# Kernel optimization log

Hardware: AMD Instinct MI355X
Metric: run time of the kernel (lower is better)

## Reference

```python
import jax, jax.numpy as jnp
from jax import lax
import numpy as np

N = 10000      # nodes
E = 160000     # edges (avg degree 16)
IN = 128       # in_channels
H = 64         # hidden_channels
OUT = 112      # out_channels
L = 28         # num GENConv layers
LN_EPS = 1e-5
MSG_EPS = 1e-7   # GENConv adds eps after relu in message
SM_EPS = 1e-16   # PyG scatter-softmax denominator eps


def _ln(x, g, b):
    mu = jnp.mean(x, axis=-1, keepdims=True)
    var = jnp.mean(jnp.square(x - mu), axis=-1, keepdims=True)
    return (x - mu) * lax.rsqrt(var + LN_EPS) * g + b


def setup_inputs() -> dict:
    key = jax.random.key(0)
    ks = jax.random.split(key, 8)

    def w(k, shape, fan_in):
        return (jax.random.normal(k, shape, dtype=jnp.float32) / np.float32(np.sqrt(fan_in)))

    x = jax.random.normal(ks[0], (N, IN), dtype=jnp.float32)
    edge_index = jax.random.randint(ks[1], (2, E), 0, N, dtype=jnp.int32)

    inp = {
        "x": x,
        "edge_index": edge_index,
        # node encoder
        "enc_W": w(ks[2], (IN, H), IN),
        "enc_b": jnp.zeros((H,), jnp.float32),
        # per-layer DeepGCNLayer LayerNorm (res+ pre-norm)
        "ln_g": jnp.ones((L, H), jnp.float32),
        "ln_b": jnp.zeros((L, H), jnp.float32),
        # per-layer learnable softmax temperature t (init 1.0)
        "t": jnp.ones((L,), jnp.float32),
        # GENConv inner MLP: Linear(H,2H) -> LayerNorm -> ReLU -> Linear(2H,H)
        "W1": w(ks[3], (L, H, 2 * H), H),
        "b1": jnp.zeros((L, 2 * H), jnp.float32),
        "mlp_g": jnp.ones((L, 2 * H), jnp.float32),
        "mlp_b": jnp.zeros((L, 2 * H), jnp.float32),
        "W2": w(ks[4], (L, 2 * H, H), 2 * H),
        "b2": jnp.zeros((L, H), jnp.float32),
        # output head
        "head_W": w(ks[5], (H, OUT), H),
        "head_b": jnp.zeros((OUT,), jnp.float32),
    }
    return inp


def reference(x, edge_index, enc_W, enc_b, ln_g, ln_b, t, W1, b1,
              mlp_g, mlp_b, W2, b2, head_W, head_b):
    src, dst = edge_index[0], edge_index[1]
    n = x.shape[0]

    h = x @ enc_W + enc_b  # node encoder

    def layer(h, params):
        lg, lb, tt, w1, bb1, mg, mb, w2, bb2 = params
        # DeepGCNLayer 'res+': norm -> act -> (dropout: identity at eval) -> conv -> residual
        z = jax.nn.relu(_ln(h, lg, lb))  # [N,H]
        # GENConv message: relu(x_j) + eps   (no edge_attr)
        m = jax.nn.relu(z[src]) + MSG_EPS  # [E,H]
        # softmax aggregation per destination node, per channel, temperature t
        logits = m * tt
        mx = jax.ops.segment_max(logits, dst, num_segments=n)  # [N,H]
        mx = jnp.where(jnp.isfinite(mx), mx, 0.0)              # empty segments
        ex = jnp.exp(logits - mx[dst])
        den = jax.ops.segment_sum(ex, dst, num_segments=n)
        alpha = ex / (den[dst] + SM_EPS)
        agg = jax.ops.segment_sum(alpha * m, dst, num_segments=n)  # [N,H]
        # GENConv: out = mlp(x_r + aggr)
        out = agg + z
        u = jax.nn.relu(_ln(out @ w1 + bb1, mg, mb))
        u = u @ w2 + bb2
        return h + u, None  # residual

    h, _ = lax.scan(layer, h, (ln_g, ln_b, t, W1, b1, mlp_g, mlp_b, W2, b2))
    return h @ head_W + head_b  # [N,OUT]
```

## Files before the change

kernel.cpp:

```cpp
#include <hip/hip_runtime.h>

#define N_NODES 10000
#define N_PAD 10016
#define N_EDGES 160000
#define IN_CH 128
#define H 64
#define H2 128
#define OUT_CH 112
#define NLAYERS 28
#define LOG2E 1.44269504088896340736f

#define GLDS16(gp, lp) __builtin_amdgcn_global_load_lds( \
    (const __attribute__((address_space(1))) void*)(gp),  \
    (__attribute__((address_space(3))) void*)(lp), 16, 0, 0)

__global__ __launch_bounds__(256) void k_count(const int* __restrict__ ei, int* __restrict__ deg) {
  int e = blockIdx.x * 256 + threadIdx.x;
  atomicAdd(&deg[ei[N_EDGES + e]], 1);
}

__global__ __launch_bounds__(1024) void k_scan(const int* __restrict__ deg, int* __restrict__ offs) {
  __shared__ int sums[1024];
  constexpr int CH = 10;
  int t = threadIdx.x;
  int base = t * CH;
  int local[CH];
  int s = 0;
  #pragma unroll
  for (int i = 0; i < CH; i++) {
    int idx = base + i;
    int v = (idx < N_NODES) ? deg[idx] : 0;
    local[i] = s; s += v;
  }
  sums[t] = s;
  __syncthreads();
  for (int off = 1; off < 1024; off <<= 1) {
    int v = (t >= off) ? sums[t - off] : 0;
    __syncthreads();
    sums[t] += v;
    __syncthreads();
  }
  int prev = (t == 0) ? 0 : sums[t - 1];
  #pragma unroll
  for (int i = 0; i < CH; i++) {
    int idx = base + i;
    if (idx < N_NODES) offs[idx] = prev + local[i];
  }
  if (t == 1023) offs[N_NODES] = sums[1023];
}

__global__ __launch_bounds__(256) void k_fill(const int* __restrict__ ei, const int* __restrict__ offs,
                                              int* __restrict__ cur, int* __restrict__ csr) {
  int e = blockIdx.x * 256 + threadIdx.x;
  int d = ei[N_EDGES + e];
  int p = offs[d] + atomicAdd(&cur[d], 1);
  csr[p] = ei[e];
}

__global__ __launch_bounds__(256) void k_pack(const float* __restrict__ W1, const float* __restrict__ W2,
                                              float* __restrict__ WP) {
  int l = blockIdx.x;
  const float* w1 = W1 + l * 8192;
  const float* w2 = W2 + l * 8192;
  float* p = WP + (size_t)l * 16384;
  int t = threadIdx.x;
  for (int i = t; i < 8192; i += 256) {
    int q = i >> 2, e = i & 3;
    int qu = q ^ ((q >> 3) & 1);
    int g = qu >> 7, lane = (qu >> 1) & 63, hh = qu & 1;
    int j = hh * 4 + e, kk = j >> 1, c = j & 1;
    p[i] = w1[(4 * g + kk) * H2 + lane * 2 + c];
  }
  for (int i = t; i < 8192; i += 256) {
    int g = i >> 8, r = i & 255;
    int lane = r >> 2, j = r & 3;
    p[8192 + i] = w2[(4 * g + j) * H + lane];
  }
}

__global__ __launch_bounds__(256) void k_encoder(
    const float* __restrict__ x, const float* __restrict__ Wenc, const float* __restrict__ benc,
    const float* __restrict__ lng, const float* __restrict__ lnb,
    float* __restrict__ h, float* __restrict__ z) {
  __shared__ float Xs[8][IN_CH];
  int t = threadIdx.x;
  int tile = blockIdx.x * 8;
  {
    int r = t >> 5, c4 = t & 31;
    float4 v = ((const float4*)x)[(tile + r) * 32 + c4];
    *(float4*)&Xs[r][c4 * 4] = v;
  }
  __syncthreads();
  int lane = t & 63;
  int wave = __builtin_amdgcn_readfirstlane(t >> 6);
  int n0 = wave * 2;
  float b = benc[lane];
  float a0 = b, a1 = b;
  #pragma unroll
  for (int k = 0; k < IN_CH; k += 4) {
    float4 X0 = *(float4*)&Xs[n0][k];
    float4 X1 = *(float4*)&Xs[n0 + 1][k];
    float w0 = Wenc[(k + 0) * H + lane];
    float w1 = Wenc[(k + 1) * H + lane];
    float w2 = Wenc[(k + 2) * H + lane];
    float w3 = Wenc[(k + 3) * H + lane];
    a0 = fmaf(X0.x, w0, a0); a0 = fmaf(X0.y, w1, a0); a0 = fmaf(X0.z, w2, a0); a0 = fmaf(X0.w, w3, a0);
    a1 = fmaf(X1.x, w0, a1); a1 = fmaf(X1.y, w1, a1); a1 = fmaf(X1.z, w2, a1); a1 = fmaf(X1.w, w3, a1);
  }
  float g = lng[lane], bb = lnb[lane];
  #pragma unroll
  for (int i = 0; i < 2; i++) {
    float a = (i == 0) ? a0 : a1;
    float s = a, q = a * a;
    #pragma unroll
    for (int m = 1; m < 64; m <<= 1) { s += __shfl_xor(s, m); q += __shfl_xor(q, m); }
    float mu = s * (1.0f / 64.0f);
    float var = q * (1.0f / 64.0f) - mu * mu;
    float rs = rsqrtf(var + 1e-5f);
    int gn = tile + n0 + i;
    h[gn * H + lane] = a;
    z[gn * H + lane] = fmaxf(fmaf((a - mu) * rs, g, bb), 0.f);
  }
}

__global__ __launch_bounds__(256, 2) void k_layer(
    const float* __restrict__ zc, float* __restrict__ zn, float* __restrict__ h,
    const int* __restrict__ offs, const int* __restrict__ csr,
    const float* __restrict__ tvec, const float* __restrict__ WP,
    const float* __restrict__ b1,
    const float* __restrict__ mg, const float* __restrict__ mb,
    const float* __restrict__ b2,
    const float* __restrict__ lngn, const float* __restrict__ lnbn,
    int l, int last) {
  __shared__ float Ws[16384];
  __shared__ float Asl[20][H];
  __shared__ float Us[20][H2];
  int t = threadIdx.x;
  int lane = t & 63;
  int wave = __builtin_amdgcn_readfirstlane(t >> 6);
  int tile = blockIdx.x * 20;
  int nb0 = tile + wave * 5;

  const float* WPl = WP + (size_t)l * 16384;
  #pragma unroll
  for (int i = 0; i < 16; i++) {
    int off = (i * 256 + t) * 4;
    GLDS16(WPl + off, Ws + off);
  }

  float tl = tvec[l] * LOG2E;
  int e0[5], e1[5];
  #pragma unroll
  for (int i = 0; i < 5; i++) { e0[i] = offs[nb0 + i]; e1[i] = offs[nb0 + i + 1]; }
  float den[5], acc[5];
  {
    int idx[5][16];
    #pragma unroll
    for (int i = 0; i < 5; i++) {
      #pragma unroll
      for (int j = 0; j < 16; j++) {
        int ee = e0[i] + j;
        int ce = ee < e1[i] ? ee : e1[i] - 1;
        idx[i][j] = csr[ce < 0 ? 0 : ce];
      }
    }
    float vv[5][16];
    #pragma unroll
    for (int i = 0; i < 5; i++)
      #pragma unroll
      for (int j = 0; j < 16; j++)
        vv[i][j] = zc[idx[i][j] * H + lane];
    #pragma unroll
    for (int i = 0; i < 5; i++) {
      den[i] = 0.f; acc[i] = 0.f;
      #pragma unroll
      for (int j = 0; j < 16; j++) {
        float v = vv[i][j] + 1e-7f;
        float pz = (e0[i] + j < e1[i]) ? exp2f(v * tl) : 0.f;
        den[i] += pz;
        acc[i] = fmaf(pz, v, acc[i]);
      }
    }
  }
  #pragma unroll
  for (int i = 0; i < 5; i++) {
    for (int base = e0[i] + 16; base < e1[i]; base += 16) {
      int id2[16]; float v2[16];
      #pragma unroll
      for (int j = 0; j < 16; j++) {
        int ee = base + j;
        id2[j] = csr[ee < e1[i] ? ee : e1[i] - 1];
      }
      #pragma unroll
      for (int j = 0; j < 16; j++)
        v2[j] = zc[id2[j] * H + lane];
      #pragma unroll
      for (int j = 0; j < 16; j++) {
        float v = v2[j] + 1e-7f;
        float pz = (base + j < e1[i]) ? exp2f(v * tl) : 0.f;
        den[i] += pz;
        acc[i] = fmaf(pz, v, acc[i]);
      }
    }
  }
  #pragma unroll
  for (int i = 0; i < 5; i++)
    Asl[wave * 5 + i][lane] = acc[i] / (den[i] + 1e-16f) + zc[(nb0 + i) * H + lane];

  __syncthreads();

  int n0 = wave * 5;
  {
    const float* b1l = b1 + l * H2;
    int c0 = lane * 2;
    float bb0 = b1l[c0], bb1 = b1l[c0 + 1];
    float u0[5], u1[5];
    #pragma unroll
    for (int i = 0; i < 5; i++) { u0[i] = bb0; u1[i] = bb1; }
    int bsw = (lane >> 2) & 1;
    #pragma unroll
    for (int g = 0; g < 16; g++) {
      float4 wa = *(float4*)&Ws[(g * 128 + lane * 2 + bsw) * 4];
      float4 wb = *(float4*)&Ws[(g * 128 + lane * 2 + 1 - bsw) * 4];
      #pragma unroll
      for (int i = 0; i < 5; i++) {
        float4 A = *(float4*)&Asl[n0 + i][g * 4];
        u0[i] = fmaf(A.x, wa.x, u0[i]); u1[i] = fmaf(A.x, wa.y, u1[i]);
        u0[i] = fmaf(A.y, wa.z, u0[i]); u1[i] = fmaf(A.y, wa.w, u1[i]);
        u0[i] = fmaf(A.z, wb.x, u0[i]); u1[i] = fmaf(A.z, wb.y, u1[i]);
        u0[i] = fmaf(A.w, wb.z, u0[i]); u1[i] = fmaf(A.w, wb.w, u1[i]);
      }
    }
    float s[5], q[5];
    #pragma unroll
    for (int i = 0; i < 5; i++) { s[i] = u0[i] + u1[i]; q[i] = u0[i] * u0[i] + u1[i] * u1[i]; }
    #pragma unroll
    for (int m = 1; m < 64; m <<= 1) {
      #pragma unroll
      for (int i = 0; i < 5; i++) { s[i] += __shfl_xor(s[i], m); q[i] += __shfl_xor(q[i], m); }
    }
    const float* mgl = mg + l * H2;
    const float* mbl = mb + l * H2;
    float g0 = mgl[c0], g1 = mgl[c0 + 1], hb0 = mbl[c0], hb1 = mbl[c0 + 1];
    #pragma unroll
    for (int i = 0; i < 5; i++) {
      float mu = s[i] * (1.0f / 128.0f);
      float rs = rsqrtf(q[i] * (1.0f / 128.0f) - mu * mu + 1e-5f);
      float o0 = fmaxf(fmaf((u0[i] - mu) * rs, g0, hb0), 0.f);
      float o1 = fmaxf(fmaf((u1[i] - mu) * rs, g1, hb1), 0.f);
      *(float2*)&Us[n0 + i][c0] = make_float2(o0, o1);
    }
  }

  {
    const float* b2l = b2 + l * H;
    float bb = b2l[lane];
    float v[5];
    #pragma unroll
    for (int i = 0; i < 5; i++) v[i] = bb;
    #pragma unroll
    for (int g = 0; g < 32; g++) {
      float4 w = *(float4*)&Ws[8192 + (g * 64 + lane) * 4];
      #pragma unroll
      for (int i = 0; i < 5; i++) {
        float4 X = *(float4*)&Us[n0 + i][g * 4];
        v[i] = fmaf(X.x, w.x, v[i]); v[i] = fmaf(X.y, w.y, v[i]);
        v[i] = fmaf(X.z, w.z, v[i]); v[i] = fmaf(X.w, w.w, v[i]);
      }
    }
    float hv[5], s[5], q[5];
    #pragma unroll
    for (int i = 0; i < 5; i++) {
      int gn = nb0 + i;
      hv[i] = h[gn * H + lane] + v[i];
      h[gn * H + lane] = hv[i];
      s[i] = hv[i]; q[i] = hv[i] * hv[i];
    }
    if (!last) {
      #pragma unroll
      for (int m = 1; m < 64; m <<= 1) {
        #pragma unroll
        for (int i = 0; i < 5; i++) { s[i] += __shfl_xor(s[i], m); q[i] += __shfl_xor(q[i], m); }
      }
      float gg = lngn[lane], gb = lnbn[lane];
      #pragma unroll
      for (int i = 0; i < 5; i++) {
        float mu = s[i] * (1.0f / 64.0f);
        float rs = rsqrtf(q[i] * (1.0f / 64.0f) - mu * mu + 1e-5f);
        zn[(nb0 + i) * H + lane] = fmaxf(fmaf((hv[i] - mu) * rs, gg, gb), 0.f);
      }
    }
  }
}

__global__ __launch_bounds__(256) void k_head(const float* __restrict__ h, const float* __restrict__ Wh,
                                              const float* __restrict__ bh, float* __restrict__ out) {
  __shared__ float Hs[8][H];
  int t = threadIdx.x;
  int tile = blockIdx.x * 8;
  if (t < 128) {
    int r = t >> 4, c4 = t & 15;
    float4 v = ((const float4*)h)[(tile + r) * 16 + c4];
    *(float4*)&Hs[r][c4 * 4] = v;
  }
  __syncthreads();
  int lane = t & 63;
  int wave = __builtin_amdgcn_readfirstlane(t >> 6);
  int n0 = wave * 2;
  int c2 = 64 + ((lane < 48) ? lane : 47);
  float b0 = bh[lane], b1 = bh[c2];
  float a00 = b0, a01 = b1, a10 = b0, a11 = b1;
  #pragma unroll
  for (int k = 0; k < H; k += 4) {
    float4 X0 = *(float4*)&Hs[n0][k];
    float4 X1 = *(float4*)&Hs[n0 + 1][k];
    float wA0 = Wh[(k + 0) * OUT_CH + lane], wB0 = Wh[(k + 0) * OUT_CH + c2];
    float wA1 = Wh[(k + 1) * OUT_CH + lane], wB1 = Wh[(k + 1) * OUT_CH + c2];
    float wA2 = Wh[(k + 2) * OUT_CH + lane], wB2 = Wh[(k + 2) * OUT_CH + c2];
    float wA3 = Wh[(k + 3) * OUT_CH + lane], wB3 = Wh[(k + 3) * OUT_CH + c2];
    a00 = fmaf(X0.x, wA0, a00); a01 = fmaf(X0.x, wB0, a01);
    a00 = fmaf(X0.y, wA1, a00); a01 = fmaf(X0.y, wB1, a01);
    a00 = fmaf(X0.z, wA2, a00); a01 = fmaf(X0.z, wB2, a01);
    a00 = fmaf(X0.w, wA3, a00); a01 = fmaf(X0.w, wB3, a01);
    a10 = fmaf(X1.x, wA0, a10); a11 = fmaf(X1.x, wB0, a11);
    a10 = fmaf(X1.y, wA1, a10); a11 = fmaf(X1.y, wB1, a11);
    a10 = fmaf(X1.z, wA2, a10); a11 = fmaf(X1.z, wB2, a11);
    a10 = fmaf(X1.w, wA3, a10); a11 = fmaf(X1.w, wB3, a11);
  }
  int gn0 = tile + n0;
  out[gn0 * OUT_CH + lane] = a00;
  out[(gn0 + 1) * OUT_CH + lane] = a10;
  if (lane < 48) {
    out[gn0 * OUT_CH + 64 + lane] = a01;
    out[(gn0 + 1) * OUT_CH + 64 + lane] = a11;
  }
}

extern "C" void kernel_launch(void* const* d_in, const int* in_sizes, int n_in,
                              void* d_out, int out_size, void* d_ws, size_t ws_size,
                              hipStream_t stream) {
  (void)in_sizes; (void)n_in; (void)out_size; (void)ws_size;
  const float* x    = (const float*)d_in[0];
  const int*   ei   = (const int*)d_in[1];
  const float* encW = (const float*)d_in[2];
  const float* encb = (const float*)d_in[3];
  const float* lng  = (const float*)d_in[4];
  const float* lnb  = (const float*)d_in[5];
  const float* tv   = (const float*)d_in[6];
  const float* W1   = (const float*)d_in[7];
  const float* b1   = (const float*)d_in[8];
  const float* mg   = (const float*)d_in[9];
  const float* mb   = (const float*)d_in[10];
  const float* W2   = (const float*)d_in[11];
  const float* b2   = (const float*)d_in[12];
  const float* Wh   = (const float*)d_in[13];
  const float* bh   = (const float*)d_in[14];

  char* ws = (char*)d_ws;
  int*   deg  = (int*)(ws + 0);
  int*   cur  = (int*)(ws + 40000);
  int*   offs = (int*)(ws + 80000);
  int*   csr  = (int*)(ws + 120064);
  float* h    = (float*)(ws + 760064);
  float* z0   = (float*)(ws + 3324160);
  float* z1   = (float*)(ws + 5888256);
  float* WP   = (float*)(ws + 8452352);

  hipMemsetAsync(ws, 0, 80000, stream);
  k_count<<<625, 256, 0, stream>>>(ei, deg);
  k_pack<<<28, 256, 0, stream>>>(W1, W2, WP);
  k_scan<<<1, 1024, 0, stream>>>(deg, offs);
  k_fill<<<625, 256, 0, stream>>>(ei, offs, cur, csr);
  k_encoder<<<1250, 256, 0, stream>>>(x, encW, encb, lng, lnb, h, z0);

  float* zc = z0;
  float* znx = z1;
  for (int l = 0; l < NLAYERS; l++) {
    int ln_next = (l + 1 < NLAYERS) ? (l + 1) : l;
    k_layer<<<500, 256, 0, stream>>>(zc, znx, h, offs, csr, tv, WP,
                                     b1, mg, mb, b2,
                                     lng + ln_next * H, lnb + ln_next * H,
                                     l, (l == NLAYERS - 1) ? 1 : 0);
    float* tmp = zc; zc = znx; znx = tmp;
  }
  k_head<<<1250, 256, 0, stream>>>(h, Wh, bh, (float*)d_out);
}
```

Baseline: 703.6 us.

## Halve layer tile to 10 nodes, stage only W1 in LDS, raise occupancy

The layer kernel now processes 10 nodes per block instead of 20 (3/3/2/2 per wave) and launches 1000 blocks. Only W1 is staged into LDS, and W2 is read directly from global, which halves the LDS footprint so launch bounds can request 4 blocks per SM. CSR indices are pre-shifted to byte offsets to save address arithmetic, and exp2f is replaced by the hardware intrinsic. The aim is more latency hiding for the gather phase, paid for with more redundant W1 loads per node and W2 reads from global or L2.

```diff
diff --git a/kernel.cpp b/kernel.cpp
--- a/kernel.cpp
+++ b/kernel.cpp
@@ -1,7 +1,6 @@
 #include <hip/hip_runtime.h>
 
 #define N_NODES 10000
-#define N_PAD 10016
 #define N_EDGES 160000
 #define IN_CH 128
 #define H 64
@@ -54,27 +53,24 @@
   int e = blockIdx.x * 256 + threadIdx.x;
   int d = ei[N_EDGES + e];
   int p = offs[d] + atomicAdd(&cur[d], 1);
-  csr[p] = ei[e];
+  csr[p] = ei[e] << 8;
 }
 
 __global__ __launch_bounds__(256) void k_pack(const float* __restrict__ W1, const float* __restrict__ W2,
-                                              float* __restrict__ WP) {
+                                              float* __restrict__ W1P, float* __restrict__ W2P) {
   int l = blockIdx.x;
-  const float* w1 = W1 + l * 8192;
-  const float* w2 = W2 + l * 8192;
-  float* p = WP + (size_t)l * 16384;
+  const float* w1 = W1 + l * 8192; float* p1 = W1P + l * 8192;
+  const float* w2 = W2 + l * 8192; float* p2 = W2P + l * 8192;
   int t = threadIdx.x;
   for (int i = t; i < 8192; i += 256) {
-    int q = i >> 2, e = i & 3;
-    int qu = q ^ ((q >> 3) & 1);
-    int g = qu >> 7, lane = (qu >> 1) & 63, hh = qu & 1;
-    int j = hh * 4 + e, kk = j >> 1, c = j & 1;
-    p[i] = w1[(4 * g + kk) * H2 + lane * 2 + c];
+    int g = i >> 9, r = i & 511;
+    int hh = r >> 8, lane = (r >> 2) & 63, e = r & 3;
+    p1[i] = w1[(4 * g + hh * 2 + (e >> 1)) * H2 + lane * 2 + (e & 1)];
   }
   for (int i = t; i < 8192; i += 256) {
     int g = i >> 8, r = i & 255;
     int lane = r >> 2, j = r & 3;
-    p[8192 + i] = w2[(4 * g + j) * H + lane];
+    p2[i] = w2[(4 * g + j) * H + lane];
   }
 }
 
@@ -123,171 +119,196 @@
   }
 }
 
-__global__ __launch_bounds__(256, 2) void k_layer(
+__global__ __launch_bounds__(256, 4) void k_layer(
     const float* __restrict__ zc, float* __restrict__ zn, float* __restrict__ h,
     const int* __restrict__ offs, const int* __restrict__ csr,
-    const float* __restrict__ tvec, const float* __restrict__ WP,
+    const float* __restrict__ tvec,
+    const float* __restrict__ W1P, const float* __restrict__ W2P,
     const float* __restrict__ b1,
     const float* __restrict__ mg, const float* __restrict__ mb,
     const float* __restrict__ b2,
     const float* __restrict__ lngn, const float* __restrict__ lnbn,
     int l, int last) {
-  __shared__ float Ws[16384];
-  __shared__ float Asl[20][H];
-  __shared__ float Us[20][H2];
+  __shared__ float Ws[8192];
+  __shared__ float Asl[10][H];
+  __shared__ float Us[10][H2];
   int t = threadIdx.x;
   int lane = t & 63;
   int wave = __builtin_amdgcn_readfirstlane(t >> 6);
-  int tile = blockIdx.x * 20;
-  int nb0 = tile + wave * 5;
-
-  const float* WPl = WP + (size_t)l * 16384;
-  #pragma unroll
-  for (int i = 0; i < 16; i++) {
+  int tile = blockIdx.x * 10;
+
+  const float* W1Pl = W1P + (size_t)l * 8192;
+  #pragma unroll
+  for (int i = 0; i < 8; i++) {
     int off = (i * 256 + t) * 4;
-    GLDS16(WPl + off, Ws + off);
-  }
+    GLDS16(W1Pl + off, Ws + off);
+  }
+
+  int s = (wave < 2) ? wave * 3 : 6 + (wave - 2) * 2;
+  int cnt = (wave < 2) ? 3 : 2;
 
   float tl = tvec[l] * LOG2E;
-  int e0[5], e1[5];
-  #pragma unroll
-  for (int i = 0; i < 5; i++) { e0[i] = offs[nb0 + i]; e1[i] = offs[nb0 + i + 1]; }
-  float den[5], acc[5];
+  int e0[3], e1[3], nd[3];
+  #pragma unroll
+  for (int i = 0; i < 3; i++) {
+    nd[i] = tile + s + ((i < cnt) ? i : cnt - 1);
+    e0[i] = offs[nd[i]]; e1[i] = offs[nd[i] + 1];
+  }
+  float den[3] = {0.f, 0.f, 0.f}, acc[3] = {0.f, 0.f, 0.f};
   {
-    int idx[5][16];
-    #pragma unroll
-    for (int i = 0; i < 5; i++) {
-      #pragma unroll
-      for (int j = 0; j < 16; j++) {
-        int ee = e0[i] + j;
-        int ce = ee < e1[i] ? ee : e1[i] - 1;
-        idx[i][j] = csr[ce < 0 ? 0 : ce];
-      }
-    }
-    float vv[5][16];
-    #pragma unroll
-    for (int i = 0; i < 5; i++)
-      #pragma unroll
-      for (int j = 0; j < 16; j++)
-        vv[i][j] = zc[idx[i][j] * H + lane];
-    #pragma unroll
-    for (int i = 0; i < 5; i++) {
-      den[i] = 0.f; acc[i] = 0.f;
-      #pragma unroll
-      for (int j = 0; j < 16; j++) {
-        float v = vv[i][j] + 1e-7f;
-        float pz = (e0[i] + j < e1[i]) ? exp2f(v * tl) : 0.f;
-        den[i] += pz;
-        acc[i] = fmaf(pz, v, acc[i]);
-      }
-    }
-  }
-  #pragma unroll
-  for (int i = 0; i < 5; i++) {
-    for (int base = e0[i] + 16; base < e1[i]; base += 16) {
-      int id2[16]; float v2[16];
-      #pragma unroll
-      for (int j = 0; j < 16; j++) {
-        int ee = base + j;
-        id2[j] = csr[ee < e1[i] ? ee : e1[i] - 1];
-      }
-      #pragma unroll
-      for (int j = 0; j < 16; j++)
-        v2[j] = zc[id2[j] * H + lane];
-      #pragma unroll
-      for (int j = 0; j < 16; j++) {
-        float v = v2[j] + 1e-7f;
-        float pz = (base + j < e1[i]) ? exp2f(v * tl) : 0.f;
-        den[i] += pz;
-        acc[i] = fmaf(pz, v, acc[i]);
-      }
-    }
-  }
-  #pragma unroll
-  for (int i = 0; i < 5; i++)
-    Asl[wave * 5 + i][lane] = acc[i] / (den[i] + 1e-16f) + zc[(nb0 + i) * H + lane];
+    int idx[3][16];
+    #pragma unroll
+    for (int i = 0; i < 3; i++) {
+      if (i < cnt) {
+        #pragma unroll
+        for (int j = 0; j < 16; j++) {
+          int ee = e0[i] + j;
+          int ce = ee < e1[i] ? ee : e1[i] - 1;
+          idx[i][j] = csr[ce < 0 ? 0 : ce];
+        }
+      }
+    }
+    float vv[3][16];
+    #pragma unroll
+    for (int i = 0; i < 3; i++) {
+      if (i < cnt) {
+        #pragma unroll
+        for (int j = 0; j < 16; j++)
+          vv[i][j] = *(const float*)((const char*)zc + idx[i][j] + (lane << 2));
+      }
+    }
+    #pragma unroll
+    for (int i = 0; i < 3; i++) {
+      if (i < cnt) {
+        #pragma unroll
+        for (int j = 0; j < 16; j++) {
+          float v = vv[i][j] + 1e-7f;
+          float pz = (e0[i] + j < e1[i]) ? __builtin_amdgcn_exp2f(v * tl) : 0.f;
+          den[i] += pz;
+          acc[i] = fmaf(pz, v, acc[i]);
+        }
+      }
+    }
+  }
+  #pragma unroll
+  for (int i = 0; i < 3; i++) {
+    if (i < cnt) {
+      for (int base = e0[i] + 16; base < e1[i]; base += 16) {
+        int id2[16]; float v2[16];
+        #pragma unroll
+        for (int j = 0; j < 16; j++) {
+          int ee = base + j;
+          id2[j] = csr[ee < e1[i] ? ee : e1[i] - 1];
+        }
+        #pragma unroll
+        for (int j = 0; j < 16; j++)
+          v2[j] = *(const float*)((const char*)zc + id2[j] + (lane << 2));
+        #pragma unroll
+        for (int j = 0; j < 16; j++) {
+          float v = v2[j] + 1e-7f;
+          float pz = (base + j < e1[i]) ? __builtin_amdgcn_exp2f(v * tl) : 0.f;
+          den[i] += pz;
+          acc[i] = fmaf(pz, v, acc[i]);
+        }
+      }
+    }
+  }
+  #pragma unroll
+  for (int i = 0; i < 3; i++) {
+    if (i < cnt) {
+      Asl[s + i][lane] = acc[i] / (den[i] + 1e-16f) + zc[nd[i] * H + lane];
+    }
+  }
 
   __syncthreads();
 
-  int n0 = wave * 5;
   {
     const float* b1l = b1 + l * H2;
     int c0 = lane * 2;
     float bb0 = b1l[c0], bb1 = b1l[c0 + 1];
-    float u0[5], u1[5];
-    #pragma unroll
-    for (int i = 0; i < 5; i++) { u0[i] = bb0; u1[i] = bb1; }
-    int bsw = (lane >> 2) & 1;
+    float u0[3], u1[3];
+    #pragma unroll
+    for (int i = 0; i < 3; i++) { u0[i] = bb0; u1[i] = bb1; }
+    int r0 = s, r1 = s + 1, r2 = s + cnt - 1;
     #pragma unroll
     for (int g = 0; g < 16; g++) {
-      float4 wa = *(float4*)&Ws[(g * 128 + lane * 2 + bsw) * 4];
-      float4 wb = *(float4*)&Ws[(g * 128 + lane * 2 + 1 - bsw) * 4];
-      #pragma unroll
-      for (int i = 0; i < 5; i++) {
-        float4 A = *(float4*)&Asl[n0 + i][g * 4];
-        u0[i] = fmaf(A.x, wa.x, u0[i]); u1[i] = fmaf(A.x, wa.y, u1[i]);
-        u0[i] = fmaf(A.y, wa.z, u0[i]); u1[i] = fmaf(A.y, wa.w, u1[i]);
-        u0[i] = fmaf(A.z, wb.x, u0[i]); u1[i] = fmaf(A.z, wb.y, u1[i]);
-        u0[i] = fmaf(A.w, wb.z, u0[i]); u1[i] = fmaf(A.w, wb.w, u1[i]);
-      }
-    }
-    float s[5], q[5];
-    #pragma unroll
-    for (int i = 0; i < 5; i++) { s[i] = u0[i] + u1[i]; q[i] = u0[i] * u0[i] + u1[i] * u1[i]; }
+      float4 wa = *(float4*)&Ws[g * 512 + lane * 4];
+      float4 wb = *(float4*)&Ws[g * 512 + 256 + lane * 4];
+      float4 A0 = *(float4*)&Asl[r0][g * 4];
+      float4 A1 = *(float4*)&Asl[r1][g * 4];
+      float4 A2 = *(float4*)&Asl[r2][g * 4];
+      u0[0] = fmaf(A0.x, wa.x, u0[0]); u1[0] = fmaf(A0.x, wa.y, u1[0]);
+      u0[0] = fmaf(A0.y, wa.z, u0[0]); u1[0] = fmaf(A0.y, wa.w, u1[0]);
+      u0[0] = fmaf(A0.z, wb.x, u0[0]); u1[0] = fmaf(A0.z, wb.y, u1[0]);
+      u0[0] = fmaf(A0.w, wb.z, u0[0]); u1[0] = fmaf(A0.w, wb.w, u1[0]);
+      u0[1] = fmaf(A1.x, wa.x, u0[1]); u1[1] = fmaf(A1.x, wa.y, u1[1]);
+      u0[1] = fmaf(A1.y, wa.z, u0[1]); u1[1] = fmaf(A1.y, wa.w, u1[1]);
+      u0[1] = fmaf(A1.z, wb.x, u0[1]); u1[1] = fmaf(A1.z, wb.y, u1[1]);
+      u0[1] = fmaf(A1.w, wb.z, u0[1]); u1[1] = fmaf(A1.w, wb.w, u1[1]);
+      u0[2] = fmaf(A2.x, wa.x, u0[2]); u1[2] = fmaf(A2.x, wa.y, u1[2]);
+      u0[2] = fmaf(A2.y, wa.z, u0[2]); u1[2] = fmaf(A2.y, wa.w, u1[2]);
+      u0[2] = fmaf(A2.z, wb.x, u0[2]); u1[2] = fmaf(A2.z, wb.y, u1[2]);
+      u0[2] = fmaf(A2.w, wb.z, u0[2]); u1[2] = fmaf(A2.w, wb.w, u1[2]);
+    }
+    float sv[3], q[3];
+    #pragma unroll
+    for (int i = 0; i < 3; i++) { sv[i] = u0[i] + u1[i]; q[i] = u0[i] * u0[i] + u1[i] * u1[i]; }
     #pragma unroll
     for (int m = 1; m < 64; m <<= 1) {
       #pragma unroll
-      for (int i = 0; i < 5; i++) { s[i] += __shfl_xor(s[i], m); q[i] += __shfl_xor(q[i], m); }
+      for (int i = 0; i < 3; i++) { sv[i] += __shfl_xor(sv[i], m); q[i] += __shfl_xor(q[i], m); }
     }
     const float* mgl = mg + l * H2;
     const float* mbl = mb + l * H2;
     float g0 = mgl[c0], g1 = mgl[c0 + 1], hb0 = mbl[c0], hb1 = mbl[c0 + 1];
     #pragma unroll
-    for (int i = 0; i < 5; i++) {
-      float mu = s[i] * (1.0f / 128.0f);
-      float rs = rsqrtf(q[i] * (1.0f / 128.0f) - mu * mu + 1e-5f);
-      float o0 = fmaxf(fmaf((u0[i] - mu) * rs, g0, hb0), 0.f);
-      float o1 = fmaxf(fmaf((u1[i] - mu) * rs, g1, hb1), 0.f);
-      *(float2*)&Us[n0 + i][c0] = make_float2(o0, o1);
+    for (int i = 0; i < 3; i++) {
+      if (i < cnt) {
+        float mu = sv[i] * (1.0f / 128.0f);
+        float rs = rsqrtf(q[i] * (1.0f / 128.0f) - mu * mu + 1e-5f);
+        float o0 = fmaxf(fmaf((u0[i] - mu) * rs, g0, hb0), 0.f);
+        float o1 = fmaxf(fmaf((u1[i] - mu) * rs, g1, hb1), 0.f);
+        *(float2*)&Us[s + i][c0] = make_float2(o0, o1);
+      }
     }
   }
 
   {
+    const float* W2Pl = W2P + (size_t)l * 8192;
     const float* b2l = b2 + l * H;
     float bb = b2l[lane];
-    float v[5];
-    #pragma unroll
-    for (int i = 0; i < 5; i++) v[i] = bb;
+    float v[3];
+    #pragma unroll
+    for (int i = 0; i < 3; i++) v[i] = bb;
+    int r0 = s, r1 = s + 1, r2 = s + cnt - 1;
     #pragma unroll
     for (int g = 0; g < 32; g++) {
-      float4 w = *(float4*)&Ws[8192 + (g * 64 + lane) * 4];
-      #pragma unroll
-      for (int i = 0; i < 5; i++) {
-        float4 X = *(float4*)&Us[n0 + i][g * 4];
-        v[i] = fmaf(X.x, w.x, v[i]); v[i] = fmaf(X.y, w.y, v[i]);
-        v[i] = fmaf(X.z, w.z, v[i]); v[i] = fmaf(X.w, w.w, v[i]);
-      }
-    }
-    float hv[5], s[5], q[5];
-    #pragma unroll
-    for (int i = 0; i < 5; i++) {
-      int gn = nb0 + i;
-      hv[i] = h[gn * H + lane] + v[i];
-      h[gn * H + lane] = hv[i];
-      s[i] = hv[i]; q[i] = hv[i] * hv[i];
-    }
-    if (!last) {
-      #pragma unroll
-      for (int m = 1; m < 64; m <<= 1) {
-        #pragma unroll
-        for (int i = 0; i < 5; i++) { s[i] += __shfl_xor(s[i], m); q[i] += __shfl_xor(q[i], m); }
-      }
-      float gg = lngn[lane], gb = lnbn[lane];
-      #pragma unroll
-      for (int i = 0; i < 5; i++) {
-        float mu = s[i] * (1.0f / 64.0f);
-        float rs = rsqrtf(q[i] * (1.0f / 64.0f) - mu * mu + 1e-5f);
-        zn[(nb0 + i) * H + lane] = fmaxf(fmaf((hv[i] - mu) * rs, gg, gb), 0.f);
+      float4 w = *(const float4*)&W2Pl[(g * 64 + lane) * 4];
+      float4 X0 = *(float4*)&Us[r0][g * 4];
+      float4 X1 = *(float4*)&Us[r1][g * 4];
+      float4 X2 = *(float4*)&Us[r2][g * 4];
+      v[0] = fmaf(X0.x, w.x, v[0]); v[0] = fmaf(X0.y, w.y, v[0]);
+      v[0] = fmaf(X0.z, w.z, v[0]); v[0] = fmaf(X0.w, w.w, v[0]);
+      v[1] = fmaf(X1.x, w.x, v[1]); v[1] = fmaf(X1.y, w.y, v[1]);
+      v[1] = fmaf(X1.z, w.z, v[1]); v[1] = fmaf(X1.w, w.w, v[1]);
+      v[2] = fmaf(X2.x, w.x, v[2]); v[2] = fmaf(X2.y, w.y, v[2]);
+      v[2] = fmaf(X2.z, w.z, v[2]); v[2] = fmaf(X2.w, w.w, v[2]);
+    }
+    float gg = lngn[lane], gb = lnbn[lane];
+    #pragma unroll
+    for (int i = 0; i < 3; i++) {
+      if (i < cnt) {
+        int gn = nd[i];
+        float hv = h[gn * H + lane] + v[i];
+        h[gn * H + lane] = hv;
+        if (!last) {
+          float sv = hv, q = hv * hv;
+          #pragma unroll
+          for (int m = 1; m < 64; m <<= 1) { sv += __shfl_xor(sv, m); q += __shfl_xor(q, m); }
+          float mu = sv * (1.0f / 64.0f);
+          float rs = rsqrtf(q * (1.0f / 64.0f) - mu * mu + 1e-5f);
+          zn[gn * H + lane] = fmaxf(fmaf((hv - mu) * rs, gg, gb), 0.f);
+        }
       }
     }
   }
@@ -362,13 +383,14 @@
   int*   offs = (int*)(ws + 80000);
   int*   csr  = (int*)(ws + 120064);
   float* h    = (float*)(ws + 760064);
-  float* z0   = (float*)(ws + 3324160);
-  float* z1   = (float*)(ws + 5888256);
-  float* WP   = (float*)(ws + 8452352);
+  float* z0   = (float*)(ws + 3320064);
+  float* z1   = (float*)(ws + 5880064);
+  float* W1P  = (float*)(ws + 8440064);
+  float* W2P  = (float*)(ws + 9357568);
 
   hipMemsetAsync(ws, 0, 80000, stream);
   k_count<<<625, 256, 0, stream>>>(ei, deg);
-  k_pack<<<28, 256, 0, stream>>>(W1, W2, WP);
+  k_pack<<<28, 256, 0, stream>>>(W1, W2, W1P, W2P);
   k_scan<<<1, 1024, 0, stream>>>(deg, offs);
   k_fill<<<625, 256, 0, stream>>>(ei, offs, cur, csr);
   k_encoder<<<1250, 256, 0, stream>>>(x, encW, encb, lng, lnb, h, z0);
@@ -377,10 +399,10 @@
   float* znx = z1;
   for (int l = 0; l < NLAYERS; l++) {
     int ln_next = (l + 1 < NLAYERS) ? (l + 1) : l;
-    k_layer<<<500, 256, 0, stream>>>(zc, znx, h, offs, csr, tv, WP,
-                                     b1, mg, mb, b2,
-                                     lng + ln_next * H, lnb + ln_next * H,
-                                     l, (l == NLAYERS - 1) ? 1 : 0);
+    k_layer<<<1000, 256, 0, stream>>>(zc, znx, h, offs, csr, tv, W1P, W2P,
+                                      b1, mg, mb, b2,
+                                      lng + ln_next * H, lnb + ln_next * H,
+                                      l, (l == NLAYERS - 1) ? 1 : 0);
     float* tmp = zc; zc = znx; znx = tmp;
   }
   k_head<<<1250, 256, 0, stream>>>(h, Wh, bh, (float*)d_out);
```

Measured after the change: 1.701 ms. 2.42x slower.
